# Kernel tuning notes

Hardware: AMD Instinct MI355X
Metric: run time of the kernel (lower is better)

The kernel has to match this reference:

```python
import jax, jax.numpy as jnp
import numpy as np

DIM = 768
HEADS = 12
HEAD_DIM = DIM // HEADS
SCALE = HEAD_DIM ** (-0.5)
GAMMA_INIT = 1.0


def _split_heads(x, B, H, Dh):
    # [B, N, C] -> [B, H, N, Dh]
    return x.reshape(B, -1, H, Dh).transpose(0, 2, 1, 3)


def setup_inputs() -> dict:
    key = jax.random.key(0)
    ks = jax.random.split(key, 10)
    B, N, C = 4, 1024, DIM
    w = lambda k: jax.random.normal(k, (C, C), dtype=jnp.float32) * 0.02
    return {
        "fc": jax.random.normal(ks[0], (B, N, C), dtype=jnp.float32),
        "fs": jax.random.normal(ks[1], (B, N, C), dtype=jnp.float32),
        "Wqc": w(ks[2]),
        "Wqs": w(ks[3]),
        "Wkc": w(ks[4]),
        "Wvc": w(ks[5]),
        "Wvs": w(ks[6]),
        "gamma": jnp.ones((HEADS,), dtype=jnp.float32) * GAMMA_INIT,
        "Wpc": w(ks[7]),
        "bpc": jnp.zeros((C,), dtype=jnp.float32),
        "Wps": w(ks[8]),
        "bps": jnp.zeros((C,), dtype=jnp.float32),
    }


def reference(fc, fs, Wqc, Wqs, Wkc, Wvc, Wvs, gamma, Wpc, bpc, Wps, bps):
    B, N, C = fc.shape
    H, Dh = HEADS, HEAD_DIM
    sg = jax.lax.stop_gradient

    qc = _split_heads(fc @ Wqc, B, H, Dh)
    qs = _split_heads(fs @ Wqs, B, H, Dh)
    kc = _split_heads(fc @ Wkc, B, H, Dh)
    vc = _split_heads(fc @ Wvc, B, H, Dh)
    vs = _split_heads(fs @ Wvs, B, H, Dh)

    # content attention: standard scaled QK^T
    attn_c = jnp.einsum("bhnd,bhmd->bhnm", qc, kc) * SCALE
    # semantic attention: L2-normalized self-similarity, per-head gamma
    qs_n = qs / jnp.linalg.norm(qs, axis=-1, keepdims=True)
    attn_s = jnp.einsum("bhnd,bhmd->bhnm", qs_n, qs_n) * gamma[None, :, None, None]

    # double softmax: identical forward values, asymmetric stop-gradients
    attn1 = jax.nn.softmax(attn_c + sg(attn_s), axis=-1)
    attn2 = jax.nn.softmax(sg(attn_c) + attn_s, axis=-1)

    oc = jnp.einsum("bhnm,bhmd->bhnd", attn1, vc).transpose(0, 2, 1, 3).reshape(B, N, C)
    os_ = jnp.einsum("bhnm,bhmd->bhnd", attn2, vs).transpose(0, 2, 1, 3).reshape(B, N, C)

    out_c = oc @ Wpc + bpc
    out_s = os_ @ Wps + bps
    return (out_c, out_s)
```

## Files before the change

### kernel.cpp

```cpp
#include <hip/hip_runtime.h>
#include <cstdint>
#include <cstddef>

#define DEV __device__ __forceinline__

typedef __bf16 v8bf __attribute__((ext_vector_type(8)));
typedef float v4f __attribute__((ext_vector_type(4)));
typedef float f32x16 __attribute__((ext_vector_type(16)));
typedef uint16_t u16;

DEV u16 f2bf(float f) {
    union { __bf16 b; u16 u; } cv;
    cv.b = (__bf16)f;
    return cv.u;
}
DEV float bf2f(u16 h) { return __uint_as_float((uint32_t)h << 16); }

DEV uint32_t pkbf(float a, float b) {
    typedef __bf16 bf2v __attribute__((ext_vector_type(2)));
    union { bf2v v; uint32_t u; } c;
    c.v = (bf2v){(__bf16)a, (__bf16)b};
    return c.u;
}

DEV void gload16(void* lds, const void* g) {
    __builtin_amdgcn_global_load_lds(
        (const __attribute__((address_space(1))) unsigned int*)g,
        (__attribute__((address_space(3))) unsigned int*)lds, 16, 0, 0);
}

__global__ __launch_bounds__(256) void k_cvt2(const float* __restrict__ a, const float* __restrict__ b,
                                              u16* __restrict__ da, u16* __restrict__ db) {
    const float* s = blockIdx.y ? b : a;
    u16* d = blockIdx.y ? db : da;
    int i = blockIdx.x * 256 + threadIdx.x;
    float4 v = reinterpret_cast<const float4*>(s)[i];
    ushort4 o;
    o.x = f2bf(v.x); o.y = f2bf(v.y); o.z = f2bf(v.z); o.w = f2bf(v.w);
    reinterpret_cast<ushort4*>(d)[i] = o;
}

__global__ __launch_bounds__(256) void k_transpose_w(
    const float* __restrict__ w0, const float* __restrict__ w1, const float* __restrict__ w2,
    const float* __restrict__ w3, const float* __restrict__ w4, const float* __restrict__ w5,
    const float* __restrict__ w6, u16* __restrict__ Wt) {
    __shared__ float tl[32][33];
    const float* W;
    switch (blockIdx.z) {
        case 0: W = w0; break; case 1: W = w1; break; case 2: W = w2; break;
        case 3: W = w3; break; case 4: W = w4; break; case 5: W = w5; break;
        default: W = w6; break;
    }
    int n0 = blockIdx.x * 32, k0 = blockIdx.y * 32;
    int tx = threadIdx.x & 31, ty = threadIdx.x >> 5;
    #pragma unroll
    for (int i = 0; i < 4; ++i)
        tl[ty + i*8][tx] = W[(size_t)(k0 + ty + i*8) * 768 + n0 + tx];
    __syncthreads();
    u16* O = Wt + (size_t)blockIdx.z * 589824;
    #pragma unroll
    for (int i = 0; i < 4; ++i)
        O[(size_t)(n0 + ty + i*8) * 768 + k0 + tx] = f2bf(tl[tx][ty + i*8]);
}

DEV void gemm_main(const u16* __restrict__ A, const u16* __restrict__ W,
                   u16* As, u16* Bs, int m0, int n0, v4f acc[4][4]) {
    const int t = threadIdx.x, lane = t & 63;
    const int wid = t >> 6, wm = wid >> 1, wn = wid & 1;
    const int lr = lane & 15, kg = lane >> 4;
    const int lrow = lane >> 3, lslot = lane & 7;
    const int s = lslot ^ lrow;
    #pragma unroll
    for (int mi = 0; mi < 4; ++mi)
        #pragma unroll
        for (int ni = 0; ni < 4; ++ni) acc[mi][ni] = (v4f){0.f, 0.f, 0.f, 0.f};
    for (int kt = 0; kt < 12; ++kt) {
        int k0 = kt * 64;
        #pragma unroll
        for (int c = 0; c < 4; ++c) {
            int rb = wid * 32 + c * 8;
            int r = rb + lrow;
            gload16((char*)As + rb * 128, A + (size_t)(m0 + r) * 768 + k0 + s * 8);
            gload16((char*)Bs + rb * 128, W + (size_t)(n0 + r) * 768 + k0 + s * 8);
        }
        __syncthreads();
        #pragma unroll
        for (int kk = 0; kk < 2; ++kk) {
            int kb2 = (kk * 32 + kg * 8) * 2;
            v8bf af[4], bfr[4];
            #pragma unroll
            for (int mi = 0; mi < 4; ++mi) {
                int rr = wm * 64 + mi * 16 + lr;
                af[mi] = *reinterpret_cast<const v8bf*>(reinterpret_cast<const char*>(As) + rr * 128 + (kb2 ^ ((rr & 7) << 4)));
            }
            #pragma unroll
            for (int ni = 0; ni < 4; ++ni) {
                int rr = wn * 64 + ni * 16 + lr;
                bfr[ni] = *reinterpret_cast<const v8bf*>(reinterpret_cast<const char*>(Bs) + rr * 128 + (kb2 ^ ((rr & 7) << 4)));
            }
            #pragma unroll
            for (int mi = 0; mi < 4; ++mi)
                #pragma unroll
                for (int ni = 0; ni < 4; ++ni)
                    acc[mi][ni] = __builtin_amdgcn_mfma_f32_16x16x32_bf16(af[mi], bfr[ni], acc[mi][ni], 0, 0, 0);
        }
        __syncthreads();
    }
}

__global__ __launch_bounds__(256) void k_gemm_proj(
    const u16* __restrict__ fcb, const u16* __restrict__ fsb, const u16* __restrict__ Wt,
    u16* __restrict__ qc, u16* __restrict__ kc, u16* __restrict__ vc,
    u16* __restrict__ qs, u16* __restrict__ vs) {
    __shared__ __align__(16) u16 As[8192], Bs[8192];
    const u16* A; const u16* W; u16* O;
    switch (blockIdx.z) {
        case 0:  A = fcb; W = Wt;              O = qc; break;
        case 1:  A = fcb; W = Wt + 589824;     O = kc; break;
        case 2:  A = fcb; W = Wt + 2 * 589824; O = vc; break;
        case 3:  A = fsb; W = Wt + 3 * 589824; O = qs; break;
        default: A = fsb; W = Wt + 4 * 589824; O = vs; break;
    }
    int m0 = blockIdx.y * 128, n0 = blockIdx.x * 128;
    v4f acc[4][4];
    gemm_main(A, W, As, Bs, m0, n0, acc);
    const int lane = threadIdx.x & 63, wid = threadIdx.x >> 6;
    const int wm = wid >> 1, wn = wid & 1, lr = lane & 15, kg = lane >> 4;
    if (blockIdx.z == 0) {
        #pragma unroll
        for (int mi = 0; mi < 4; ++mi)
            #pragma unroll
            for (int ni = 0; ni < 4; ++ni)
                #pragma unroll
                for (int r = 0; r < 4; ++r) acc[mi][ni][r] *= 0.18033688f;
    } else if (blockIdx.z == 3) {
        #pragma unroll
        for (int mi = 0; mi < 4; ++mi)
            #pragma unroll
            for (int r = 0; r < 4; ++r) {
                float ss = 0.f;
                #pragma unroll
                for (int ni = 0; ni < 4; ++ni) ss += acc[mi][ni][r] * acc[mi][ni][r];
                ss += __shfl_xor(ss, 1); ss += __shfl_xor(ss, 2);
                ss += __shfl_xor(ss, 4); ss += __shfl_xor(ss, 8);
                float rs = rsqrtf(ss);
                #pragma unroll
                for (int ni = 0; ni < 4; ++ni) acc[mi][ni][r] *= rs;
            }
    }
    #pragma unroll
    for (int mi = 0; mi < 4; ++mi)
        #pragma unroll
        for (int ni = 0; ni < 4; ++ni)
            #pragma unroll
            for (int r = 0; r < 4; ++r) {
                int rowg = m0 + wm * 64 + mi * 16 + kg * 4 + r;
                int colg = n0 + wn * 64 + ni * 16 + lr;
                O[(size_t)rowg * 768 + colg] = f2bf(acc[mi][ni][r]);
            }
}

__global__ __launch_bounds__(256) void k_gemm_out(
    const u16* __restrict__ ocb, const u16* __restrict__ osb, const u16* __restrict__ Wt,
    const float* __restrict__ bpc, const float* __restrict__ bps, float* __restrict__ out) {
    __shared__ __align__(16) u16 As[8192], Bs[8192];
    const u16* A; const u16* W; const float* bias; float* O;
    if (blockIdx.z == 0) { A = ocb; W = Wt + 5 * 589824; bias = bpc; O = out; }
    else                 { A = osb; W = Wt + 6 * 589824; bias = bps; O = out + 3145728; }
    int m0 = blockIdx.y * 128, n0 = blockIdx.x * 128;
    v4f acc[4][4];
    gemm_main(A, W, As, Bs, m0, n0, acc);
    const int lane = threadIdx.x & 63, wid = threadIdx.x >> 6;
    const int wm = wid >> 1, wn = wid & 1, lr = lane & 15, kg = lane >> 4;
    #pragma unroll
    for (int mi = 0; mi < 4; ++mi)
        #pragma unroll
        for (int ni = 0; ni < 4; ++ni)
            #pragma unroll
            for (int r = 0; r < 4; ++r) {
                int rowg = m0 + wm * 64 + mi * 16 + kg * 4 + r;
                int colg = n0 + wn * 64 + ni * 16 + lr;
                O[(size_t)rowg * 768 + colg] = acc[mi][ni][r] + bias[colg];
            }
}

__global__ __launch_bounds__(256) void k_transpose_v(
    const u16* __restrict__ vc, const u16* __restrict__ vs,
    u16* __restrict__ vcT, u16* __restrict__ vsT) {
    __shared__ u16 tile[64][65];
    const u16* src = blockIdx.z ? vs : vc;
    u16* dst = blockIdx.z ? vsT : vcT;
    int bh = blockIdx.y, b = bh / 12, h = bh % 12;
    int n0 = blockIdx.x * 64;
    int t = threadIdx.x;
    #pragma unroll
    for (int i = 0; i < 16; ++i) {
        int idx = i * 256 + t, n = idx >> 6, d = idx & 63;
        tile[n][d] = src[(size_t)(b * 1024 + n0 + n) * 768 + h * 64 + d];
    }
    __syncthreads();
    #pragma unroll
    for (int i = 0; i < 16; ++i) {
        int idx = i * 256 + t, d = idx >> 6, n = idx & 63;
        dst[(size_t)(bh * 64 + d) * 1024 + n0 + n] = tile[n][d];
    }
}

__global__ __launch_bounds__(256, 2) void k_attn(
    const u16* __restrict__ qc, const u16* __restrict__ kc, const u16* __restrict__ qsn,
    const u16* __restrict__ vcT, const u16* __restrict__ vsT,
    const float* __restrict__ gamma,
    u16* __restrict__ oc, u16* __restrict__ os) {
    __shared__ __align__(16) u16 KQ[2][4][4096];
    const int t = threadIdx.x, lane = t & 63, w = t >> 6;
    const int lq = lane & 31, hf = lane >> 5;
    const int qg = w >> 1, kvh = w & 1;
    const int lrow = lane >> 3, lslot = lane & 7;
    const int sslot = lslot ^ lrow;

    int lin = blockIdx.y * 16 + blockIdx.x;
    int swz = (lin & 7) * 96 + (lin >> 3);
    const int qb = swz & 15, bh = swz >> 4;
    const int b = bh / 12, h = bh % 12;
    const float gam = gamma[h] * 1.44269504088896340736f;

    const u16* gb; size_t rstride, kmul;
    switch (w) {
        case 0:  gb = kc  + (size_t)b * 786432 + h * 64; rstride = 768;  kmul = 768; break;
        case 1:  gb = qsn + (size_t)b * 786432 + h * 64; rstride = 768;  kmul = 768; break;
        case 2:  gb = vcT + (size_t)bh * 65536;          rstride = 1024; kmul = 1;   break;
        default: gb = vsT + (size_t)bh * 65536;          rstride = 1024; kmul = 1;   break;
    }

    const u16* qp1 = qc  + (size_t)(b * 1024 + qb * 64 + qg * 32 + lq) * 768 + h * 64 + hf * 8;
    const u16* qp2 = qsn + (size_t)(b * 1024 + qb * 64 + qg * 32 + lq) * 768 + h * 64 + hf * 8;
    v8bf qcB[4], qsB[4];
    #pragma unroll
    for (int s = 0; s < 4; ++s) {
        qcB[s] = *reinterpret_cast<const v8bf*>(qp1 + s * 16);
        qsB[s] = *reinterpret_cast<const v8bf*>(qp2 + s * 16);
    }

    f32x16 ocA[2], osA[2];
    #pragma unroll
    for (int dt = 0; dt < 2; ++dt) {
        #pragma unroll
        for (int r = 0; r < 16; ++r) { ocA[dt][r] = 0.f; osA[dt][r] = 0.f; }
    }
    float lsum = 0.f;

    {
        char* ld = (char*)KQ[0][w];
        #pragma unroll
        for (int c = 0; c < 8; ++c) {
            int r = c * 8 + lrow;
            gload16(ld + c * 1024, gb + (size_t)r * rstride + sslot * 8);
        }
    }
    __syncthreads();

    int cur = 0;
    for (int tile = 0; tile < 16; ++tile) {
        if (tile < 15) {
            size_t kv1 = (size_t)(tile + 1) * 64;
            char* ld = (char*)KQ[cur ^ 1][w];
            #pragma unroll
            for (int c = 0; c < 8; ++c) {
                int r = c * 8 + lrow;
                gload16(ld + c * 1024, gb + kv1 * kmul + (size_t)r * rstride + sslot * 8);
            }
        }
        const char* K_s  = (const char*)KQ[cur][0];
        const char* Q2_s = (const char*)KQ[cur][1];
        const char* Vc_s = (const char*)KQ[cur][2];
        const char* Vs_s = (const char*)KQ[cur][3];

        f32x16 ac, as;
        #pragma unroll
        for (int r = 0; r < 16; ++r) { ac[r] = 0.f; as[r] = 0.f; }
        const int rowA = kvh * 32 + lq;
        __builtin_amdgcn_s_setprio(1);
        #pragma unroll
        for (int s = 0; s < 4; ++s) {
            int colb = s * 32 + hf * 16;
            int off = rowA * 128 + (colb ^ ((rowA & 7) << 4));
            v8bf kf  = *reinterpret_cast<const v8bf*>(K_s + off);
            v8bf q2f = *reinterpret_cast<const v8bf*>(Q2_s + off);
            ac = __builtin_amdgcn_mfma_f32_32x32x16_bf16(kf,  qcB[s], ac, 0, 0, 0);
            as = __builtin_amdgcn_mfma_f32_32x32x16_bf16(q2f, qsB[s], as, 0, 0, 0);
        }
        __builtin_amdgcn_s_setprio(0);

        float p[16];
        #pragma unroll
        for (int r = 0; r < 16; ++r)
            p[r] = __builtin_exp2f(fmaf(gam, as[r], ac[r]));
        lsum += ((p[0]+p[1])+(p[2]+p[3])) + ((p[4]+p[5])+(p[6]+p[7]))
              + ((p[8]+p[9])+(p[10]+p[11])) + ((p[12]+p[13])+(p[14]+p[15]));

        uint32_t A0 = pkbf(p[0], p[1]),  A1 = pkbf(p[2], p[3]);
        uint32_t A2 = pkbf(p[4], p[5]),  A3 = pkbf(p[6], p[7]);
        uint32_t A4 = pkbf(p[8], p[9]),  A5 = pkbf(p[10], p[11]);
        uint32_t A6 = pkbf(p[12], p[13]), A7 = pkbf(p[14], p[15]);
        uint32_t pay0 = hf ? A0 : A2;
        uint32_t pay1 = hf ? A1 : A3;
        uint32_t rec0 = (uint32_t)__shfl_xor((int)pay0, 32);
        uint32_t rec1 = (uint32_t)__shfl_xor((int)pay1, 32);
        uint32_t w0 = hf ? rec0 : A0;
        uint32_t w1 = hf ? rec1 : A1;
        uint32_t w2 = hf ? A2 : rec0;
        uint32_t w3 = hf ? A3 : rec1;
        uint32_t pay2 = hf ? A4 : A6;
        uint32_t pay3 = hf ? A5 : A7;
        uint32_t rec2 = (uint32_t)__shfl_xor((int)pay2, 32);
        uint32_t rec3 = (uint32_t)__shfl_xor((int)pay3, 32);
        uint32_t w4 = hf ? rec2 : A4;
        uint32_t w5 = hf ? rec3 : A5;
        uint32_t w6 = hf ? A6 : rec2;
        uint32_t w7 = hf ? A7 : rec3;
        union { uint32_t u[4]; v8bf v; } pa0, pa1;
        pa0.u[0] = w0; pa0.u[1] = w1; pa0.u[2] = w2; pa0.u[3] = w3;
        pa1.u[0] = w4; pa1.u[1] = w5; pa1.u[2] = w6; pa1.u[3] = w7;

        __builtin_amdgcn_s_setprio(1);
        #pragma unroll
        for (int dt = 0; dt < 2; ++dt) {
            int rowV = dt * 32 + lq;
            #pragma unroll
            for (int s = 0; s < 2; ++s) {
                int colb = kvh * 64 + s * 32 + hf * 16;
                int off = rowV * 128 + (colb ^ ((rowV & 7) << 4));
                v8bf vcf = *reinterpret_cast<const v8bf*>(Vc_s + off);
                v8bf vsf = *reinterpret_cast<const v8bf*>(Vs_s + off);
                v8bf ap = s ? pa1.v : pa0.v;
                ocA[dt] = __builtin_amdgcn_mfma_f32_32x32x16_bf16(ap, vcf, ocA[dt], 0, 0, 0);
                osA[dt] = __builtin_amdgcn_mfma_f32_32x32x16_bf16(ap, vsf, osA[dt], 0, 0, 0);
            }
        }
        __builtin_amdgcn_s_setprio(0);

        __syncthreads();
        cur ^= 1;
    }

    lsum += __shfl_xor(lsum, 32);
    float* red   = reinterpret_cast<float*>(&KQ[0][0][0]);
    float* red_l = red;
    float* red_o = red + 64;
    if (kvh == 1) {
        if (lane < 32) red_l[qg * 32 + lq] = lsum;
        #pragma unroll
        for (int st = 0; st < 2; ++st)
            #pragma unroll
            for (int dt = 0; dt < 2; ++dt)
                #pragma unroll
                for (int r = 0; r < 16; ++r) {
                    int idx = st * 32 + dt * 16 + r;
                    float v = st ? osA[dt][r] : ocA[dt][r];
                    red_o[(qg * 64 + idx) * 64 + lane] = v;
                }
    }
    __syncthreads();
    if (kvh == 0) {
        float ltot = lsum + red_l[qg * 32 + lq];
        float rl = 1.0f / ltot;
        if (lane < 32) red_l[qg * 32 + lq] = rl;
        #pragma unroll
        for (int st = 0; st < 2; ++st)
            #pragma unroll
            for (int dt = 0; dt < 2; ++dt)
                #pragma unroll
                for (int r = 0; r < 16; ++r) {
                    int rowq = (r & 3) + 8 * (r >> 2) + 4 * hf;
                    float rlv = red_l[qg * 32 + rowq];
                    int idx = st * 32 + dt * 16 + r;
                    float own = st ? osA[dt][r] : ocA[dt][r];
                    float v = (own + red_o[(qg * 64 + idx) * 64 + lane]) * rlv;
                    u16* dst = st ? os : oc;
                    dst[(size_t)(b * 1024 + qb * 64 + qg * 32 + rowq) * 768 + h * 64 + dt * 32 + lq] = f2bf(v);
                }
    }
}

extern "C" void kernel_launch(void* const* d_in, const int* in_sizes, int n_in,
                              void* d_out, int out_size, void* d_ws, size_t ws_size,
                              hipStream_t stream) {
    const float* fc    = (const float*)d_in[0];
    const float* fs    = (const float*)d_in[1];
    const float* Wqc   = (const float*)d_in[2];
    const float* Wqs   = (const float*)d_in[3];
    const float* Wkc   = (const float*)d_in[4];
    const float* Wvc   = (const float*)d_in[5];
    const float* Wvs   = (const float*)d_in[6];
    const float* gamma = (const float*)d_in[7];
    const float* Wpc   = (const float*)d_in[8];
    const float* bpc   = (const float*)d_in[9];
    const float* Wps   = (const float*)d_in[10];
    const float* bps   = (const float*)d_in[11];
    float* out = (float*)d_out;

    const size_t NT = 3145728;
    u16* ws  = (u16*)d_ws;
    u16* fcb = ws;
    u16* fsb = fcb + NT;
    u16* Wt  = fsb + NT;
    u16* qc  = Wt + (size_t)7 * 589824;
    u16* kc  = qc + NT;
    u16* vc  = kc + NT;
    u16* qs  = vc + NT;
    u16* vs  = qs + NT;
    u16* vcT = vs + NT;
    u16* vsT = vcT + NT;
    u16* ocb = fcb;
    u16* osb = fsb;

    k_cvt2<<<dim3(3072, 2), 256, 0, stream>>>(fc, fs, fcb, fsb);
    k_transpose_w<<<dim3(24, 24, 7), 256, 0, stream>>>(Wqc, Wkc, Wvc, Wqs, Wvs, Wpc, Wps, Wt);
    k_gemm_proj<<<dim3(6, 32, 5), 256, 0, stream>>>(fcb, fsb, Wt, qc, kc, vc, qs, vs);
    k_transpose_v<<<dim3(16, 48, 2), 256, 0, stream>>>(vc, vs, vcT, vsT);
    k_attn<<<dim3(16, 48), 256, 0, stream>>>(qc, kc, qs, vcT, vsT, gamma, ocb, osb);
    k_gemm_out<<<dim3(6, 32, 2), 256, 0, stream>>>(ocb, osb, Wt, bpc, bps, out);
}
```

Baseline: 127.3 us.

## Single-buffer K/Q2 tiles in LDS with mid-iteration reload to shrink shared memory

Changes the attention kernel's LDS plan so the K and normalized-Q tiles are single-buffered. Their next-tile loads are issued after a mid-iteration barrier, once the QK MFMAs have consumed them, while the V tiles stay double-buffered. This cuts LDS from 64KB to 48KB per block, which may allow more resident blocks. The cost is an extra barrier per tile and less latency hiding for the K/Q2 loads, which now overlap only the softmax and PV phase. __syncthreads is replaced with explicit vmcnt waits plus s_barrier.

```diff
diff --git a/kernel.cpp b/kernel.cpp
--- a/kernel.cpp
+++ b/kernel.cpp
@@ -27,6 +27,11 @@
     __builtin_amdgcn_global_load_lds(
         (const __attribute__((address_space(1))) unsigned int*)g,
         (__attribute__((address_space(3))) unsigned int*)lds, 16, 0, 0);
+}
+
+DEV void wait_vm0() {
+    asm volatile("s_waitcnt vmcnt(0)" ::: "memory");
+    __builtin_amdgcn_sched_barrier(0);
 }
 
 __global__ __launch_bounds__(256) void k_cvt2(const float* __restrict__ a, const float* __restrict__ b,
@@ -211,7 +216,10 @@
     const u16* __restrict__ vcT, const u16* __restrict__ vsT,
     const float* __restrict__ gamma,
     u16* __restrict__ oc, u16* __restrict__ os) {
-    __shared__ __align__(16) u16 KQ[2][4][4096];
+    __shared__ __align__(16) u16 SH[24576];
+    u16* K_s8  = SH;
+    u16* Q2_s8 = SH + 4096;
+    u16* Vb    = SH + 8192;
     const int t = threadIdx.x, lane = t & 63, w = t >> 6;
     const int lq = lane & 31, hf = lane >> 5;
     const int qg = w >> 1, kvh = w & 1;
@@ -231,6 +239,7 @@
         case 2:  gb = vcT + (size_t)bh * 65536;          rstride = 1024; kmul = 1;   break;
         default: gb = vsT + (size_t)bh * 65536;          rstride = 1024; kmul = 1;   break;
     }
+    u16* fixdst = (w == 0) ? K_s8 : Q2_s8;
 
     const u16* qp1 = qc  + (size_t)(b * 1024 + qb * 64 + qg * 32 + lq) * 768 + h * 64 + hf * 8;
     const u16* qp2 = qsn + (size_t)(b * 1024 + qb * 64 + qg * 32 + lq) * 768 + h * 64 + hf * 8;
@@ -250,30 +259,31 @@
     float lsum = 0.f;
 
     {
-        char* ld = (char*)KQ[0][w];
+        char* ld = (w < 2) ? (char*)fixdst : (char*)(Vb + (w - 2) * 4096);
         #pragma unroll
         for (int c = 0; c < 8; ++c) {
             int r = c * 8 + lrow;
             gload16(ld + c * 1024, gb + (size_t)r * rstride + sslot * 8);
         }
     }
-    __syncthreads();
+    wait_vm0();
+    __builtin_amdgcn_s_barrier();
 
     int cur = 0;
     for (int tile = 0; tile < 16; ++tile) {
-        if (tile < 15) {
+        if (tile < 15 && w >= 2) {
             size_t kv1 = (size_t)(tile + 1) * 64;
-            char* ld = (char*)KQ[cur ^ 1][w];
+            char* ld = (char*)(Vb + ((cur ^ 1) * 2 + (w - 2)) * 4096);
             #pragma unroll
             for (int c = 0; c < 8; ++c) {
                 int r = c * 8 + lrow;
                 gload16(ld + c * 1024, gb + kv1 * kmul + (size_t)r * rstride + sslot * 8);
             }
         }
-        const char* K_s  = (const char*)KQ[cur][0];
-        const char* Q2_s = (const char*)KQ[cur][1];
-        const char* Vc_s = (const char*)KQ[cur][2];
-        const char* Vs_s = (const char*)KQ[cur][3];
+        const char* K_s  = (const char*)K_s8;
+        const char* Q2_s = (const char*)Q2_s8;
+        const char* Vc_s = (const char*)(Vb + (cur * 2 + 0) * 4096);
+        const char* Vs_s = (const char*)(Vb + (cur * 2 + 1) * 4096);
 
         f32x16 ac, as;
         #pragma unroll
@@ -290,6 +300,16 @@
             as = __builtin_amdgcn_mfma_f32_32x32x16_bf16(q2f, qsB[s], as, 0, 0, 0);
         }
         __builtin_amdgcn_s_setprio(0);
+
+        __builtin_amdgcn_s_barrier();
+        if (tile < 15 && w < 2) {
+            size_t kv1 = (size_t)(tile + 1) * 64;
+            #pragma unroll
+            for (int c = 0; c < 8; ++c) {
+                int r = c * 8 + lrow;
+                gload16((char*)fixdst + c * 1024, gb + kv1 * kmul + (size_t)r * rstride + sslot * 8);
+            }
+        }
 
         float p[16];
         #pragma unroll
@@ -339,12 +359,13 @@
         }
         __builtin_amdgcn_s_setprio(0);
 
-        __syncthreads();
+        wait_vm0();
+        __builtin_amdgcn_s_barrier();
         cur ^= 1;
     }
 
     lsum += __shfl_xor(lsum, 32);
-    float* red   = reinterpret_cast<float*>(&KQ[0][0][0]);
+    float* red   = reinterpret_cast<float*>(SH);
     float* red_l = red;
     float* red_o = red + 64;
     if (kvh == 1) {
```

Measured after the change: 127.3 us. About the same (-0.0%).

## Enlarge attention block to 128 queries and merge prep kernels into one launch

Applied to the files above, without the earlier changes.

The attention kernel now runs 512 threads per block covering 128 query rows, so each K/Q/V tile loaded into shared memory serves twice as many queries. Each pair of waves splits the global-to-LDS load of one array. The epilogue reduction reuses the same LDS in two passes (content, then semantic) so it fits the unchanged shared buffer. Separately, the input conversion and weight transpose kernels are fused into a single launch. The 512-thread block with launch_bounds(512,2) may limit registers per thread and cause spills, and the extra syncs add cost to the epilogue.

```diff
diff --git a/kernel.cpp b/kernel.cpp
--- a/kernel.cpp
+++ b/kernel.cpp
@@ -14,7 +14,6 @@
     cv.b = (__bf16)f;
     return cv.u;
 }
-DEV float bf2f(u16 h) { return __uint_as_float((uint32_t)h << 16); }
 
 DEV uint32_t pkbf(float a, float b) {
     typedef __bf16 bf2v __attribute__((ext_vector_type(2)));
@@ -29,35 +28,40 @@
         (__attribute__((address_space(3))) unsigned int*)lds, 16, 0, 0);
 }
 
-__global__ __launch_bounds__(256) void k_cvt2(const float* __restrict__ a, const float* __restrict__ b,
-                                              u16* __restrict__ da, u16* __restrict__ db) {
-    const float* s = blockIdx.y ? b : a;
-    u16* d = blockIdx.y ? db : da;
-    int i = blockIdx.x * 256 + threadIdx.x;
-    float4 v = reinterpret_cast<const float4*>(s)[i];
-    ushort4 o;
-    o.x = f2bf(v.x); o.y = f2bf(v.y); o.z = f2bf(v.z); o.w = f2bf(v.w);
-    reinterpret_cast<ushort4*>(d)[i] = o;
-}
-
-__global__ __launch_bounds__(256) void k_transpose_w(
+__global__ __launch_bounds__(256) void k_prep(
+    const float* __restrict__ fc, const float* __restrict__ fs,
+    u16* __restrict__ fcb, u16* __restrict__ fsb,
     const float* __restrict__ w0, const float* __restrict__ w1, const float* __restrict__ w2,
     const float* __restrict__ w3, const float* __restrict__ w4, const float* __restrict__ w5,
     const float* __restrict__ w6, u16* __restrict__ Wt) {
     __shared__ float tl[32][33];
+    int bid = blockIdx.x;
+    if (bid < 6144) {
+        const float* s = (bid < 3072) ? fc : fs;
+        u16* d = (bid < 3072) ? fcb : fsb;
+        int blk = (bid < 3072) ? bid : (bid - 3072);
+        int i = blk * 256 + threadIdx.x;
+        float4 v = reinterpret_cast<const float4*>(s)[i];
+        ushort4 o;
+        o.x = f2bf(v.x); o.y = f2bf(v.y); o.z = f2bf(v.z); o.w = f2bf(v.w);
+        reinterpret_cast<ushort4*>(d)[i] = o;
+        return;
+    }
+    int tid = bid - 6144;
+    int z = tid / 576, rem = tid % 576;
     const float* W;
-    switch (blockIdx.z) {
+    switch (z) {
         case 0: W = w0; break; case 1: W = w1; break; case 2: W = w2; break;
         case 3: W = w3; break; case 4: W = w4; break; case 5: W = w5; break;
         default: W = w6; break;
     }
-    int n0 = blockIdx.x * 32, k0 = blockIdx.y * 32;
+    int n0 = (rem % 24) * 32, k0 = (rem / 24) * 32;
     int tx = threadIdx.x & 31, ty = threadIdx.x >> 5;
     #pragma unroll
     for (int i = 0; i < 4; ++i)
         tl[ty + i*8][tx] = W[(size_t)(k0 + ty + i*8) * 768 + n0 + tx];
     __syncthreads();
-    u16* O = Wt + (size_t)blockIdx.z * 589824;
+    u16* O = Wt + (size_t)z * 589824;
     #pragma unroll
     for (int i = 0; i < 4; ++i)
         O[(size_t)(n0 + ty + i*8) * 768 + k0 + tx] = f2bf(tl[tx][ty + i*8]);
@@ -206,7 +210,7 @@
     }
 }
 
-__global__ __launch_bounds__(256, 2) void k_attn(
+__global__ __launch_bounds__(512, 2) void k_attn(
     const u16* __restrict__ qc, const u16* __restrict__ kc, const u16* __restrict__ qsn,
     const u16* __restrict__ vcT, const u16* __restrict__ vsT,
     const float* __restrict__ gamma,
@@ -215,25 +219,26 @@
     const int t = threadIdx.x, lane = t & 63, w = t >> 6;
     const int lq = lane & 31, hf = lane >> 5;
     const int qg = w >> 1, kvh = w & 1;
+    const int arr = w >> 1, half = w & 1;
     const int lrow = lane >> 3, lslot = lane & 7;
     const int sslot = lslot ^ lrow;
 
-    int lin = blockIdx.y * 16 + blockIdx.x;
-    int swz = (lin & 7) * 96 + (lin >> 3);
-    const int qb = swz & 15, bh = swz >> 4;
+    int lin = blockIdx.y * 8 + blockIdx.x;
+    int swz = (lin & 7) * 48 + (lin >> 3);
+    const int qb = swz & 7, bh = swz >> 3;
     const int b = bh / 12, h = bh % 12;
     const float gam = gamma[h] * 1.44269504088896340736f;
 
     const u16* gb; size_t rstride, kmul;
-    switch (w) {
+    switch (arr) {
         case 0:  gb = kc  + (size_t)b * 786432 + h * 64; rstride = 768;  kmul = 768; break;
         case 1:  gb = qsn + (size_t)b * 786432 + h * 64; rstride = 768;  kmul = 768; break;
         case 2:  gb = vcT + (size_t)bh * 65536;          rstride = 1024; kmul = 1;   break;
         default: gb = vsT + (size_t)bh * 65536;          rstride = 1024; kmul = 1;   break;
     }
 
-    const u16* qp1 = qc  + (size_t)(b * 1024 + qb * 64 + qg * 32 + lq) * 768 + h * 64 + hf * 8;
-    const u16* qp2 = qsn + (size_t)(b * 1024 + qb * 64 + qg * 32 + lq) * 768 + h * 64 + hf * 8;
+    const u16* qp1 = qc  + (size_t)(b * 1024 + qb * 128 + qg * 32 + lq) * 768 + h * 64 + hf * 8;
+    const u16* qp2 = qsn + (size_t)(b * 1024 + qb * 128 + qg * 32 + lq) * 768 + h * 64 + hf * 8;
     v8bf qcB[4], qsB[4];
     #pragma unroll
     for (int s = 0; s < 4; ++s) {
@@ -250,10 +255,10 @@
     float lsum = 0.f;
 
     {
-        char* ld = (char*)KQ[0][w];
-        #pragma unroll
-        for (int c = 0; c < 8; ++c) {
-            int r = c * 8 + lrow;
+        char* ld = (char*)KQ[0][arr] + half * 4096;
+        #pragma unroll
+        for (int c = 0; c < 4; ++c) {
+            int r = half * 32 + c * 8 + lrow;
             gload16(ld + c * 1024, gb + (size_t)r * rstride + sslot * 8);
         }
     }
@@ -263,10 +268,10 @@
     for (int tile = 0; tile < 16; ++tile) {
         if (tile < 15) {
             size_t kv1 = (size_t)(tile + 1) * 64;
-            char* ld = (char*)KQ[cur ^ 1][w];
-            #pragma unroll
-            for (int c = 0; c < 8; ++c) {
-                int r = c * 8 + lrow;
+            char* ld = (char*)KQ[cur ^ 1][arr] + half * 4096;
+            #pragma unroll
+            for (int c = 0; c < 4; ++c) {
+                int r = half * 32 + c * 8 + lrow;
                 gload16(ld + c * 1024, gb + kv1 * kmul + (size_t)r * rstride + sslot * 8);
             }
         }
@@ -346,19 +351,14 @@
     lsum += __shfl_xor(lsum, 32);
     float* red   = reinterpret_cast<float*>(&KQ[0][0][0]);
     float* red_l = red;
-    float* red_o = red + 64;
+    float* red_o = red + 128;
     if (kvh == 1) {
         if (lane < 32) red_l[qg * 32 + lq] = lsum;
         #pragma unroll
-        for (int st = 0; st < 2; ++st)
-            #pragma unroll
-            for (int dt = 0; dt < 2; ++dt)
-                #pragma unroll
-                for (int r = 0; r < 16; ++r) {
-                    int idx = st * 32 + dt * 16 + r;
-                    float v = st ? osA[dt][r] : ocA[dt][r];
-                    red_o[(qg * 64 + idx) * 64 + lane] = v;
-                }
+        for (int dt = 0; dt < 2; ++dt)
+            #pragma unroll
+            for (int r = 0; r < 16; ++r)
+                red_o[(qg * 32 + dt * 16 + r) * 64 + lane] = ocA[dt][r];
     }
     __syncthreads();
     if (kvh == 0) {
@@ -366,19 +366,34 @@
         float rl = 1.0f / ltot;
         if (lane < 32) red_l[qg * 32 + lq] = rl;
         #pragma unroll
-        for (int st = 0; st < 2; ++st)
-            #pragma unroll
-            for (int dt = 0; dt < 2; ++dt)
-                #pragma unroll
-                for (int r = 0; r < 16; ++r) {
-                    int rowq = (r & 3) + 8 * (r >> 2) + 4 * hf;
-                    float rlv = red_l[qg * 32 + rowq];
-                    int idx = st * 32 + dt * 16 + r;
-                    float own = st ? osA[dt][r] : ocA[dt][r];
-                    float v = (own + red_o[(qg * 64 + idx) * 64 + lane]) * rlv;
-                    u16* dst = st ? os : oc;
-                    dst[(size_t)(b * 1024 + qb * 64 + qg * 32 + rowq) * 768 + h * 64 + dt * 32 + lq] = f2bf(v);
-                }
+        for (int dt = 0; dt < 2; ++dt)
+            #pragma unroll
+            for (int r = 0; r < 16; ++r) {
+                int rowq = (r & 3) + 8 * (r >> 2) + 4 * hf;
+                float rlv = red_l[qg * 32 + rowq];
+                float v = (ocA[dt][r] + red_o[(qg * 32 + dt * 16 + r) * 64 + lane]) * rlv;
+                oc[(size_t)(b * 1024 + qb * 128 + qg * 32 + rowq) * 768 + h * 64 + dt * 32 + lq] = f2bf(v);
+            }
+    }
+    __syncthreads();
+    if (kvh == 1) {
+        #pragma unroll
+        for (int dt = 0; dt < 2; ++dt)
+            #pragma unroll
+            for (int r = 0; r < 16; ++r)
+                red_o[(qg * 32 + dt * 16 + r) * 64 + lane] = osA[dt][r];
+    }
+    __syncthreads();
+    if (kvh == 0) {
+        #pragma unroll
+        for (int dt = 0; dt < 2; ++dt)
+            #pragma unroll
+            for (int r = 0; r < 16; ++r) {
+                int rowq = (r & 3) + 8 * (r >> 2) + 4 * hf;
+                float rlv = red_l[qg * 32 + rowq];
+                float v = (osA[dt][r] + red_o[(qg * 32 + dt * 16 + r) * 64 + lane]) * rlv;
+                os[(size_t)(b * 1024 + qb * 128 + qg * 32 + rowq) * 768 + h * 64 + dt * 32 + lq] = f2bf(v);
+            }
     }
 }
 
@@ -414,10 +429,9 @@
     u16* ocb = fcb;
     u16* osb = fsb;
 
-    k_cvt2<<<dim3(3072, 2), 256, 0, stream>>>(fc, fs, fcb, fsb);
-    k_transpose_w<<<dim3(24, 24, 7), 256, 0, stream>>>(Wqc, Wkc, Wvc, Wqs, Wvs, Wpc, Wps, Wt);
+    k_prep<<<10176, 256, 0, stream>>>(fc, fs, fcb, fsb, Wqc, Wkc, Wvc, Wqs, Wvs, Wpc, Wps, Wt);
     k_gemm_proj<<<dim3(6, 32, 5), 256, 0, stream>>>(fcb, fsb, Wt, qc, kc, vc, qs, vs);
     k_transpose_v<<<dim3(16, 48, 2), 256, 0, stream>>>(vc, vs, vcT, vsT);
-    k_attn<<<dim3(16, 48), 256, 0, stream>>>(qc, kc, qs, vcT, vsT, gamma, ocb, osb);
+    k_attn<<<dim3(8, 48), 512, 0, stream>>>(qc, kc, qs, vcT, vsT, gamma, ocb, osb);
     k_gemm_out<<<dim3(6, 32, 2), 256, 0, stream>>>(ocb, osb, Wt, bpc, bps, out);
 }
```

New measurement: 132.2 us. 1.04x slower.
